# Performance work log

Hardware: AMD Instinct MI355X
Metric: run time of the kernel (lower is better)

Reference implementation:

```python
import jax, jax.numpy as jnp
import numpy as np

B, N, C, H = 8, 1024, 768, 12
DH = C // H


def setup_inputs() -> dict:
    key = jax.random.key(0)
    k1, k2, k3, k4 = jax.random.split(key, 4)
    x = jax.random.normal(k1, (B, N, C), dtype=jnp.float32)
    mask = jax.random.randint(k2, (B, N), 0, 2, dtype=jnp.int32)
    # torch Linear weights stored transposed; build directly as (in, out)
    w_qkv = jax.random.normal(k3, (C, 3 * C), dtype=jnp.float32) * (C ** -0.5)
    w_proj = jax.random.normal(k4, (C, C), dtype=jnp.float32) * (C ** -0.5)
    b_proj = jnp.zeros((C,), dtype=jnp.float32)
    return {"x": x, "mask": mask, "w_qkv": w_qkv, "w_proj": w_proj, "b_proj": b_proj}


def reference(x, mask, w_qkv, w_proj, b_proj):
    scale = DH ** -0.5
    qkv = (x @ w_qkv).reshape(B, N, 3, H, DH)          # (B,N,3,H,Dh)
    q, k, v = jnp.moveaxis(qkv, 2, 0)                  # each (B,N,H,Dh)
    q = q.transpose(0, 2, 1, 3)                        # (B,H,N,Dh)
    k = k.transpose(0, 2, 1, 3)
    v = v.transpose(0, 2, 1, 3)
    attn = jnp.einsum('bhqd,bhkd->bhqk', q, k) * scale  # (B,H,N,N)
    # mask (B,N) masks key positions for all queries/heads
    attn = jnp.where(mask[:, None, None, :] != 0, -jnp.inf, attn)
    attn = jax.nn.softmax(attn, axis=-1)
    out = jnp.einsum('bhqk,bhkd->bhqd', attn, v)        # (B,H,N,Dh)
    out = out.transpose(0, 2, 1, 3).reshape(B, N, C)
    return out @ w_proj + b_proj
```

## Files before the change

### kernel.cpp

```cpp
#include <hip/hip_runtime.h>
#include <cstdint>
#include <cstddef>

#define Bb   8
#define Nn   1024
#define Ccn  768
#define Hh   12
#define DHn  64
#define Mrows (Bb * Nn)
#define N3C  (3 * Ccn)
#define BHn  (Bb * Hh)

typedef __attribute__((ext_vector_type(8))) short bf16x8;
typedef __attribute__((ext_vector_type(4))) float f32x4;

static __device__ __forceinline__ unsigned short f2bf(float f) {
    unsigned int u = __builtin_bit_cast(unsigned int, f);
    return (unsigned short)((u + 0x7FFFu + ((u >> 16) & 1u)) >> 16);
}
static __device__ __forceinline__ float bf2f(unsigned short s) {
    unsigned int u = ((unsigned int)s) << 16;
    return __builtin_bit_cast(float, u);
}
static __device__ __forceinline__ unsigned pack2bf(float a, float b) {
    unsigned ua = __builtin_bit_cast(unsigned, a) + 0x8000u;
    unsigned ub = __builtin_bit_cast(unsigned, b) + 0x8000u;
    return (ua >> 16) | (ub & 0xFFFF0000u);
}
static __device__ __forceinline__ void glds16(const void* g, void* l) {
    __builtin_amdgcn_global_load_lds((const __attribute__((address_space(1))) void*)g,
                                     (__attribute__((address_space(3))) void*)l,
                                     16, 0, 0);
}

__global__ void convert_x_mask_kernel(const float* __restrict__ x,
                                      unsigned short* __restrict__ xb,
                                      const int* __restrict__ mask,
                                      float* __restrict__ maskneg, int n8) {
    int i = blockIdx.x * blockDim.x + threadIdx.x;
    if (i < Mrows) maskneg[i] = (mask[i] != 0) ? -1.0e9f : 0.0f;
    if (i >= n8) return;
    const f32x4* xp = (const f32x4*)x;
    f32x4 a = xp[2 * i], b = xp[2 * i + 1];
    bf16x8 v;
#pragma unroll
    for (int j = 0; j < 4; ++j) {
        v[j]     = (short)f2bf(a[j]);
        v[4 + j] = (short)f2bf(b[j]);
    }
    ((bf16x8*)xb)[i] = v;
}

__global__ void transpose_w2_kernel(const float* __restrict__ Wqkv,
                                    unsigned short* __restrict__ WqkvT,
                                    const float* __restrict__ Wproj,
                                    unsigned short* __restrict__ WprojT) {
    __shared__ float tile[32][33];
    int xb = blockIdx.x;
    const float* W; unsigned short* WT; int C;
    if (xb < 72) { W = Wqkv;  WT = WqkvT;  C = N3C; }
    else         { W = Wproj; WT = WprojT; C = Ccn; xb -= 72; }
    const int R = Ccn;
    const int c0 = xb * 32, r0 = blockIdx.y * 32;
    const int tx = threadIdx.x, ty = threadIdx.y;
#pragma unroll
    for (int i = 0; i < 4; ++i)
        tile[ty + i * 8][tx] = W[(size_t)(r0 + ty + i * 8) * C + c0 + tx];
    __syncthreads();
#pragma unroll
    for (int i = 0; i < 4; ++i)
        WT[(size_t)(c0 + ty + i * 8) * R + r0 + tx] = f2bf(tile[tx][ty + i * 8]);
}

__global__ void transpose_v_kernel(const unsigned short* __restrict__ vb,
                                   unsigned short* __restrict__ vtb) {
    __shared__ unsigned short tile[32][34];
    const int bh = blockIdx.z;
    const int d0 = blockIdx.x * 32, n0 = blockIdx.y * 32;
    const int tx = threadIdx.x, ty = threadIdx.y;
    const unsigned short* src = vb + (size_t)bh * Nn * DHn;
    unsigned short* dst = vtb + (size_t)bh * DHn * Nn;
#pragma unroll
    for (int i = 0; i < 4; ++i)
        tile[ty + i * 8][tx] = src[(size_t)(n0 + ty + i * 8) * DHn + d0 + tx];
    __syncthreads();
#pragma unroll
    for (int i = 0; i < 4; ++i)
        dst[(size_t)(d0 + ty + i * 8) * Nn + n0 + tx] = tile[tx][ty + i * 8];
}

__global__ __launch_bounds__(256) void gemm_qkv_kernel(
    const unsigned short* __restrict__ A,
    const unsigned short* __restrict__ BT,
    unsigned short* __restrict__ qkvb) {
    constexpr int K = Ccn;
    const int bm = blockIdx.x, bn = blockIdx.y;
    const int t = threadIdx.x, wv = t >> 6, l = t & 63;
    const int fr = l & 15, quad = l >> 4;
    const int wm = (wv >> 1) * 64, wn = (wv & 1) * 64;
    __shared__ __align__(16) unsigned short As[128 * 32];
    __shared__ __align__(16) unsigned short Bs[128 * 32];
    const f32x4 zero = {0.f, 0.f, 0.f, 0.f};
    f32x4 acc[4][4];
#pragma unroll
    for (int i = 0; i < 4; ++i)
#pragma unroll
        for (int j = 0; j < 4; ++j) acc[i][j] = zero;

    const int srow = wv * 16 + (l >> 2);
    const int scol_dst = (l & 3) * 8;
    const int scol_src = (((l & 3) ^ ((srow >> 1) & 3)) << 3);
    const unsigned short* Ag = A + (size_t)(bm * 128 + srow) * K + scol_src;
    const unsigned short* Bg = BT + (size_t)(bn * 128 + srow) * K + scol_src;
    unsigned short* Al = &As[srow * 32 + scol_dst];
    unsigned short* Bl = &Bs[srow * 32 + scol_dst];
    const int rsw = ((fr >> 1) & 3);

    for (int k0 = 0; k0 < K; k0 += 32) {
        glds16(Ag, Al);
        glds16(Ag + (size_t)64 * K, Al + 64 * 32);
        glds16(Bg, Bl);
        glds16(Bg + (size_t)64 * K, Bl + 64 * 32);
        Ag += 32; Bg += 32;
        __syncthreads();
        bf16x8 af[4], bfv[4];
#pragma unroll
        for (int i = 0; i < 4; ++i)
            af[i] = *(const bf16x8*)&As[(wm + i * 16 + fr) * 32 + ((quad ^ rsw) << 3)];
#pragma unroll
        for (int i = 0; i < 4; ++i)
            bfv[i] = *(const bf16x8*)&Bs[(wn + i * 16 + fr) * 32 + ((quad ^ rsw) << 3)];
#pragma unroll
        for (int i = 0; i < 4; ++i)
#pragma unroll
            for (int j = 0; j < 4; ++j)
                acc[i][j] = __builtin_amdgcn_mfma_f32_16x16x32_bf16(af[i], bfv[j], acc[i][j], 0, 0, 0);
        __syncthreads();
    }
#pragma unroll
    for (int j = 0; j < 4; ++j) {
        int col = bn * 128 + wn + j * 16 + fr;
        int s = col / Ccn;
        int rem = col - s * Ccn;
        int hh = rem >> 6, d = rem & 63;
#pragma unroll
        for (int i = 0; i < 4; ++i) {
#pragma unroll
            for (int r = 0; r < 4; ++r) {
                int row = bm * 128 + wm + i * 16 + quad * 4 + r;
                int b = row >> 10, nq = row & 1023;
                qkvb[((((size_t)s * Bb + b) * Hh + hh) * Nn + nq) * DHn + d] = f2bf(acc[i][j][r]);
            }
        }
    }
}

__global__ __launch_bounds__(256) void gemm_proj_kernel(
    const unsigned short* __restrict__ A,
    const unsigned short* __restrict__ BT,
    const float* __restrict__ bias,
    float* __restrict__ out) {
    constexpr int K = Ccn;
    const int bm = blockIdx.x, bn = blockIdx.y;
    const int t = threadIdx.x, wv = t >> 6, l = t & 63;
    const int fr = l & 15, quad = l >> 4;
    const int wm = (wv >> 1) * 64, wn = (wv & 1) * 32;
    __shared__ __align__(16) unsigned short As[128 * 32];
    __shared__ __align__(16) unsigned short Bs[64 * 32];
    const f32x4 zero = {0.f, 0.f, 0.f, 0.f};
    f32x4 acc[4][2];
#pragma unroll
    for (int i = 0; i < 4; ++i)
#pragma unroll
        for (int j = 0; j < 2; ++j) acc[i][j] = zero;

    const int srow = wv * 16 + (l >> 2);
    const int scol_dst = (l & 3) * 8;
    const int scol_src = (((l & 3) ^ ((srow >> 1) & 3)) << 3);
    const unsigned short* Ag = A + (size_t)(bm * 128 + srow) * K + scol_src;
    unsigned short* Al = &As[srow * 32 + scol_dst];
    const int rB = t >> 2, cB = t & 3;
    const int bsrc = ((cB ^ ((rB >> 1) & 3)) << 3);
    const unsigned short* Bg = BT + (size_t)(bn * 64 + rB) * K + bsrc;
    unsigned short* Bl = &Bs[rB * 32 + cB * 8];
    const int rsw = ((fr >> 1) & 3);

    for (int k0 = 0; k0 < K; k0 += 32) {
        glds16(Ag, Al);
        glds16(Ag + (size_t)64 * K, Al + 64 * 32);
        glds16(Bg, Bl);
        Ag += 32; Bg += 32;
        __syncthreads();
        bf16x8 af[4], bfv[2];
#pragma unroll
        for (int i = 0; i < 4; ++i)
            af[i] = *(const bf16x8*)&As[(wm + i * 16 + fr) * 32 + ((quad ^ rsw) << 3)];
#pragma unroll
        for (int j = 0; j < 2; ++j)
            bfv[j] = *(const bf16x8*)&Bs[(wn + j * 16 + fr) * 32 + ((quad ^ rsw) << 3)];
#pragma unroll
        for (int i = 0; i < 4; ++i)
#pragma unroll
            for (int j = 0; j < 2; ++j)
                acc[i][j] = __builtin_amdgcn_mfma_f32_16x16x32_bf16(af[i], bfv[j], acc[i][j], 0, 0, 0);
        __syncthreads();
    }
#pragma unroll
    for (int j = 0; j < 2; ++j) {
        int col = bn * 64 + wn + j * 16 + fr;
        float bv = bias[col];
#pragma unroll
        for (int i = 0; i < 4; ++i) {
#pragma unroll
            for (int r = 0; r < 4; ++r) {
                int row = bm * 128 + wm + i * 16 + quad * 4 + r;
                out[(size_t)row * Ccn + col] = acc[i][j][r] + bv;
            }
        }
    }
}

__global__ __launch_bounds__(256, 3) void attn_fused(
    const unsigned short* __restrict__ qkvb,
    const unsigned short* __restrict__ vtb,
    const float* __restrict__ maskneg,
    unsigned short* __restrict__ attnb) {
    const int hb = blockIdx.x, qt = blockIdx.y;
    const int b = hb / Hh, h = hb - b * Hh;
    const int t = threadIdx.x, wv = t >> 6, l = t & 63;
    const int fr = l & 15, quad = l >> 4;
    __shared__ __align__(16) unsigned short Ks[2][64 * 64];
    __shared__ __align__(16) unsigned short VTs[2][64 * 64];
    __shared__ __align__(16) float Ms[2][64];
    __shared__ __align__(16) unsigned short Pbuf[4][16 * 72];
    const size_t bh = (size_t)b * Hh + h;
    const unsigned short* Qg = qkvb + bh * (Nn * DHn);
    const unsigned short* Kg = qkvb + (BHn + bh) * (Nn * DHn);
    const unsigned short* Vg = vtb + bh * (DHn * Nn);
    const float* Mg = maskneg + b * Nn;
    const int q0 = qt * 128 + wv * 32;

    bf16x8 qf[2][2];
#pragma unroll
    for (int g = 0; g < 2; ++g)
#pragma unroll
        for (int c = 0; c < 2; ++c) {
            bf16x8 raw = *(const bf16x8*)&Qg[(size_t)(q0 + g * 16 + fr) * DHn + c * 32 + quad * 8];
            bf16x8 sc;
#pragma unroll
            for (int j = 0; j < 8; ++j)
                sc[j] = (short)f2bf(bf2f((unsigned short)raw[j]) * 0.125f);
            qf[g][c] = sc;
        }
    const f32x4 zero = {0.f, 0.f, 0.f, 0.f};
    f32x4 o[2][4];
    float rs[2] = {0.f, 0.f};
#pragma unroll
    for (int g = 0; g < 2; ++g)
#pragma unroll
        for (int r = 0; r < 4; ++r) o[g][r] = zero;

    const int srow = wv * 8 + (l >> 3);
    const int lincol = (l & 7) * 8;
    const int swzcol = (((l & 7) ^ (srow & 7)) << 3);

    auto stage = [&](int kbase, int bsel) {
        glds16(&Kg[(size_t)(kbase + srow) * DHn + swzcol], &Ks[bsel][srow * 64 + lincol]);
        glds16(&Kg[(size_t)(kbase + srow + 32) * DHn + swzcol], &Ks[bsel][(srow + 32) * 64 + lincol]);
        glds16(&Vg[(size_t)srow * Nn + kbase + swzcol], &VTs[bsel][srow * 64 + lincol]);
        glds16(&Vg[(size_t)(srow + 32) * Nn + kbase + swzcol], &VTs[bsel][(srow + 32) * 64 + lincol]);
        if (t < 16) glds16(&Mg[kbase + t * 4], &Ms[bsel][t * 4]);
    };
    auto compute = [&](int bsel) {
        f32x4 ci[4];
#pragma unroll
        for (int kt = 0; kt < 4; ++kt)
            ci[kt] = *(const f32x4*)&Ms[bsel][kt * 16 + quad * 4];
        bf16x8 kf0[4], kf1[4];
#pragma unroll
        for (int kt = 0; kt < 4; ++kt) {
            int rr = kt * 16 + fr, sw = rr & 7;
            kf0[kt] = *(const bf16x8*)&Ks[bsel][rr * 64 + ((quad ^ sw) << 3)];
            kf1[kt] = *(const bf16x8*)&Ks[bsel][rr * 64 + (((quad + 4) ^ sw) << 3)];
        }
        f32x4 sg[2][4];
#pragma unroll
        for (int g = 0; g < 2; ++g)
#pragma unroll
            for (int kt = 0; kt < 4; ++kt) {
                f32x4 s = __builtin_amdgcn_mfma_f32_16x16x32_bf16(kf0[kt], qf[g][0], ci[kt], 0, 0, 0);
                sg[g][kt] = __builtin_amdgcn_mfma_f32_16x16x32_bf16(kf1[kt], qf[g][1], s, 0, 0, 0);
            }
        bf16x8 vf0[4], vf1[4];
#pragma unroll
        for (int dt = 0; dt < 4; ++dt) {
            int rr = dt * 16 + fr, sw = rr & 7;
            vf0[dt] = *(const bf16x8*)&VTs[bsel][rr * 64 + ((quad ^ sw) << 3)];
            vf1[dt] = *(const bf16x8*)&VTs[bsel][rr * 64 + (((quad + 4) ^ sw) << 3)];
        }
        unsigned short* Pw = Pbuf[wv];
#pragma unroll
        for (int g = 0; g < 2; ++g) {
#pragma unroll
            for (int kt = 0; kt < 4; ++kt) {
                float p0 = __expf(sg[g][kt][0]);
                float p1 = __expf(sg[g][kt][1]);
                float p2 = __expf(sg[g][kt][2]);
                float p3 = __expf(sg[g][kt][3]);
                rs[g] += (p0 + p1) + (p2 + p3);
                uint2 pk;
                pk.x = pack2bf(p0, p1);
                pk.y = pack2bf(p2, p3);
                *(uint2*)&Pw[fr * 72 + kt * 16 + quad * 4] = pk;
            }
            bf16x8 pa0 = *(const bf16x8*)&Pw[fr * 72 + quad * 8];
            bf16x8 pa1 = *(const bf16x8*)&Pw[fr * 72 + 32 + quad * 8];
#pragma unroll
            for (int dt = 0; dt < 4; ++dt) {
                f32x4 t0 = __builtin_amdgcn_mfma_f32_16x16x32_bf16(pa0, vf0[dt], o[g][dt], 0, 0, 0);
                o[g][dt] = __builtin_amdgcn_mfma_f32_16x16x32_bf16(pa1, vf1[dt], t0, 0, 0, 0);
            }
        }
    };

    stage(0, 0);
    __syncthreads();
    for (int r = 0; r < 16; ++r) {
        if (r < 15) stage((r + 1) * 64, (r + 1) & 1);
        compute(r & 1);
        __syncthreads();
    }
#pragma unroll
    for (int g = 0; g < 2; ++g) {
        float r2 = rs[g] + __shfl_xor(rs[g], 16, 64);
        float rfull = r2 + __shfl_xor(r2, 32, 64);
        float inv[4];
#pragma unroll
        for (int r = 0; r < 4; ++r) {
            float lv = __shfl(rfull, quad * 4 + r, 64);
            inv[r] = (lv > 0.f) ? 1.0f / lv : 0.f;
        }
#pragma unroll
        for (int dt = 0; dt < 4; ++dt)
#pragma unroll
            for (int r = 0; r < 4; ++r) {
                int q = q0 + g * 16 + quad * 4 + r;
                attnb[((size_t)(b * Nn + q) * Hh + h) * DHn + dt * 16 + fr] = f2bf(o[g][dt][r] * inv[r]);
            }
    }
}

#define OFF_XB     0u
#define OFF_WQKVT  12582912u
#define OFF_WPROJT 16121856u
#define OFF_MASKB  17301504u
#define OFF_QKVB   17334272u
#define OFF_VTB    55083008u
#define OFF_ATTNB  67665920u

extern "C" void kernel_launch(void* const* d_in, const int* in_sizes, int n_in,
                              void* d_out, int out_size, void* d_ws, size_t ws_size,
                              hipStream_t stream) {
    const float* x      = (const float*)d_in[0];
    const int*   mask   = (const int*)d_in[1];
    const float* w_qkv  = (const float*)d_in[2];
    const float* w_proj = (const float*)d_in[3];
    const float* b_proj = (const float*)d_in[4];
    float* out = (float*)d_out;
    char* ws = (char*)d_ws;
    unsigned short* xb     = (unsigned short*)(ws + OFF_XB);
    unsigned short* wqkvT  = (unsigned short*)(ws + OFF_WQKVT);
    unsigned short* wprojT = (unsigned short*)(ws + OFF_WPROJT);
    float*          maskng = (float*)(ws + OFF_MASKB);
    unsigned short* qkvb   = (unsigned short*)(ws + OFF_QKVB);
    unsigned short* vtb    = (unsigned short*)(ws + OFF_VTB);
    unsigned short* attnb  = (unsigned short*)(ws + OFF_ATTNB);

    convert_x_mask_kernel<<<dim3(3072), dim3(256), 0, stream>>>(x, xb, mask, maskng, Mrows * Ccn / 8);
    transpose_w2_kernel<<<dim3(96, 24), dim3(32, 8), 0, stream>>>(w_qkv, wqkvT, w_proj, wprojT);
    gemm_qkv_kernel<<<dim3(Mrows / 128, N3C / 128), dim3(256), 0, stream>>>(xb, wqkvT, qkvb);
    transpose_v_kernel<<<dim3(DHn / 32, Nn / 32, BHn), dim3(32, 8), 0, stream>>>(
        qkvb + (size_t)2 * BHn * Nn * DHn, vtb);
    attn_fused<<<dim3(BHn, Nn / 128), dim3(256), 0, stream>>>(qkvb, vtb, maskng, attnb);
    gemm_proj_kernel<<<dim3(Mrows / 128, Ccn / 64), dim3(256), 0, stream>>>(attnb, wprojT, b_proj, out);
}
```

Measured before the change: 192.4 us.

## Double-buffer LDS tiles in both GEMMs and merge prep kernels into one launch

Both bf16 GEMMs now keep two LDS buffers per operand. The async global-to-LDS load for the next K-slice is issued before the MFMA work on the current slice, so memory latency can overlap with compute and only one barrier per iteration remains. The x/mask conversion and the weight transpose/convert kernels are merged into a single launch to save one kernel launch. The cost is twice the LDS per GEMM block, which may lower occupancy.

```diff
diff --git a/kernel.cpp b/kernel.cpp
--- a/kernel.cpp
+++ b/kernel.cpp
@@ -33,36 +33,38 @@
                                      16, 0, 0);
 }
 
-__global__ void convert_x_mask_kernel(const float* __restrict__ x,
-                                      unsigned short* __restrict__ xb,
-                                      const int* __restrict__ mask,
-                                      float* __restrict__ maskneg, int n8) {
-    int i = blockIdx.x * blockDim.x + threadIdx.x;
-    if (i < Mrows) maskneg[i] = (mask[i] != 0) ? -1.0e9f : 0.0f;
-    if (i >= n8) return;
-    const f32x4* xp = (const f32x4*)x;
-    f32x4 a = xp[2 * i], b = xp[2 * i + 1];
-    bf16x8 v;
-#pragma unroll
-    for (int j = 0; j < 4; ++j) {
-        v[j]     = (short)f2bf(a[j]);
-        v[4 + j] = (short)f2bf(b[j]);
-    }
-    ((bf16x8*)xb)[i] = v;
-}
-
-__global__ void transpose_w2_kernel(const float* __restrict__ Wqkv,
-                                    unsigned short* __restrict__ WqkvT,
-                                    const float* __restrict__ Wproj,
-                                    unsigned short* __restrict__ WprojT) {
+__global__ void prep_kernel(const float* __restrict__ x,
+                            unsigned short* __restrict__ xb,
+                            const int* __restrict__ mask,
+                            float* __restrict__ maskneg,
+                            const float* __restrict__ Wqkv,
+                            unsigned short* __restrict__ WqkvT,
+                            const float* __restrict__ Wproj,
+                            unsigned short* __restrict__ WprojT) {
     __shared__ float tile[32][33];
-    int xb = blockIdx.x;
+    int bx = blockIdx.x;
+    if (bx < 3072) {
+        int i = bx * 256 + threadIdx.x;
+        if (i < Mrows) maskneg[i] = (mask[i] != 0) ? -1.0e9f : 0.0f;
+        const f32x4* xp = (const f32x4*)x;
+        f32x4 a = xp[2 * i], b = xp[2 * i + 1];
+        bf16x8 v;
+#pragma unroll
+        for (int j = 0; j < 4; ++j) {
+            v[j]     = (short)f2bf(a[j]);
+            v[4 + j] = (short)f2bf(b[j]);
+        }
+        ((bf16x8*)xb)[i] = v;
+        return;
+    }
+    bx -= 3072;
+    int xt = bx % 96, yt = bx / 96;
     const float* W; unsigned short* WT; int C;
-    if (xb < 72) { W = Wqkv;  WT = WqkvT;  C = N3C; }
-    else         { W = Wproj; WT = WprojT; C = Ccn; xb -= 72; }
+    if (xt < 72) { W = Wqkv;  WT = WqkvT;  C = N3C; }
+    else         { W = Wproj; WT = WprojT; C = Ccn; xt -= 72; }
     const int R = Ccn;
-    const int c0 = xb * 32, r0 = blockIdx.y * 32;
-    const int tx = threadIdx.x, ty = threadIdx.y;
+    const int c0 = xt * 32, r0 = yt * 32;
+    const int tx = threadIdx.x & 31, ty = threadIdx.x >> 5;
 #pragma unroll
     for (int i = 0; i < 4; ++i)
         tile[ty + i * 8][tx] = W[(size_t)(r0 + ty + i * 8) * C + c0 + tx];
@@ -98,8 +100,8 @@
     const int t = threadIdx.x, wv = t >> 6, l = t & 63;
     const int fr = l & 15, quad = l >> 4;
     const int wm = (wv >> 1) * 64, wn = (wv & 1) * 64;
-    __shared__ __align__(16) unsigned short As[128 * 32];
-    __shared__ __align__(16) unsigned short Bs[128 * 32];
+    __shared__ __align__(16) unsigned short As[2][128 * 32];
+    __shared__ __align__(16) unsigned short Bs[2][128 * 32];
     const f32x4 zero = {0.f, 0.f, 0.f, 0.f};
     f32x4 acc[4][4];
 #pragma unroll
@@ -112,24 +114,30 @@
     const int scol_src = (((l & 3) ^ ((srow >> 1) & 3)) << 3);
     const unsigned short* Ag = A + (size_t)(bm * 128 + srow) * K + scol_src;
     const unsigned short* Bg = BT + (size_t)(bn * 128 + srow) * K + scol_src;
-    unsigned short* Al = &As[srow * 32 + scol_dst];
-    unsigned short* Bl = &Bs[srow * 32 + scol_dst];
+    const int ldst = srow * 32 + scol_dst;
     const int rsw = ((fr >> 1) & 3);
 
-    for (int k0 = 0; k0 < K; k0 += 32) {
-        glds16(Ag, Al);
-        glds16(Ag + (size_t)64 * K, Al + 64 * 32);
-        glds16(Bg, Bl);
-        glds16(Bg + (size_t)64 * K, Bl + 64 * 32);
-        Ag += 32; Bg += 32;
-        __syncthreads();
+    auto stage = [&](int r, int bsel) {
+        const unsigned short* Ar = Ag + r * 32;
+        const unsigned short* Br = Bg + r * 32;
+        glds16(Ar, &As[bsel][ldst]);
+        glds16(Ar + (size_t)64 * K, &As[bsel][ldst + 64 * 32]);
+        glds16(Br, &Bs[bsel][ldst]);
+        glds16(Br + (size_t)64 * K, &Bs[bsel][ldst + 64 * 32]);
+    };
+    stage(0, 0);
+    __syncthreads();
+    for (int r = 0; r < 24; ++r) {
+        if (r < 23) stage(r + 1, (r + 1) & 1);
+        const unsigned short* Asb = As[r & 1];
+        const unsigned short* Bsb = Bs[r & 1];
         bf16x8 af[4], bfv[4];
 #pragma unroll
         for (int i = 0; i < 4; ++i)
-            af[i] = *(const bf16x8*)&As[(wm + i * 16 + fr) * 32 + ((quad ^ rsw) << 3)];
+            af[i] = *(const bf16x8*)&Asb[(wm + i * 16 + fr) * 32 + ((quad ^ rsw) << 3)];
 #pragma unroll
         for (int i = 0; i < 4; ++i)
-            bfv[i] = *(const bf16x8*)&Bs[(wn + i * 16 + fr) * 32 + ((quad ^ rsw) << 3)];
+            bfv[i] = *(const bf16x8*)&Bsb[(wn + i * 16 + fr) * 32 + ((quad ^ rsw) << 3)];
 #pragma unroll
         for (int i = 0; i < 4; ++i)
 #pragma unroll
@@ -165,8 +173,8 @@
     const int t = threadIdx.x, wv = t >> 6, l = t & 63;
     const int fr = l & 15, quad = l >> 4;
     const int wm = (wv >> 1) * 64, wn = (wv & 1) * 32;
-    __shared__ __align__(16) unsigned short As[128 * 32];
-    __shared__ __align__(16) unsigned short Bs[64 * 32];
+    __shared__ __align__(16) unsigned short As[2][128 * 32];
+    __shared__ __align__(16) unsigned short Bs[2][64 * 32];
     const f32x4 zero = {0.f, 0.f, 0.f, 0.f};
     f32x4 acc[4][2];
 #pragma unroll
@@ -178,26 +186,32 @@
     const int scol_dst = (l & 3) * 8;
     const int scol_src = (((l & 3) ^ ((srow >> 1) & 3)) << 3);
     const unsigned short* Ag = A + (size_t)(bm * 128 + srow) * K + scol_src;
-    unsigned short* Al = &As[srow * 32 + scol_dst];
+    const int ldstA = srow * 32 + scol_dst;
     const int rB = t >> 2, cB = t & 3;
     const int bsrc = ((cB ^ ((rB >> 1) & 3)) << 3);
     const unsigned short* Bg = BT + (size_t)(bn * 64 + rB) * K + bsrc;
-    unsigned short* Bl = &Bs[rB * 32 + cB * 8];
+    const int ldstB = rB * 32 + cB * 8;
     const int rsw = ((fr >> 1) & 3);
 
-    for (int k0 = 0; k0 < K; k0 += 32) {
-        glds16(Ag, Al);
-        glds16(Ag + (size_t)64 * K, Al + 64 * 32);
-        glds16(Bg, Bl);
-        Ag += 32; Bg += 32;
-        __syncthreads();
+    auto stage = [&](int r, int bsel) {
+        const unsigned short* Ar = Ag + r * 32;
+        glds16(Ar, &As[bsel][ldstA]);
+        glds16(Ar + (size_t)64 * K, &As[bsel][ldstA + 64 * 32]);
+        glds16(Bg + r * 32, &Bs[bsel][ldstB]);
+    };
+    stage(0, 0);
+    __syncthreads();
+    for (int r = 0; r < 24; ++r) {
+        if (r < 23) stage(r + 1, (r + 1) & 1);
+        const unsigned short* Asb = As[r & 1];
+        const unsigned short* Bsb = Bs[r & 1];
         bf16x8 af[4], bfv[2];
 #pragma unroll
         for (int i = 0; i < 4; ++i)
-            af[i] = *(const bf16x8*)&As[(wm + i * 16 + fr) * 32 + ((quad ^ rsw) << 3)];
+            af[i] = *(const bf16x8*)&Asb[(wm + i * 16 + fr) * 32 + ((quad ^ rsw) << 3)];
 #pragma unroll
         for (int j = 0; j < 2; ++j)
-            bfv[j] = *(const bf16x8*)&Bs[(wn + j * 16 + fr) * 32 + ((quad ^ rsw) << 3)];
+            bfv[j] = *(const bf16x8*)&Bsb[(wn + j * 16 + fr) * 32 + ((quad ^ rsw) << 3)];
 #pragma unroll
         for (int i = 0; i < 4; ++i)
 #pragma unroll
@@ -376,8 +390,8 @@
     unsigned short* vtb    = (unsigned short*)(ws + OFF_VTB);
     unsigned short* attnb  = (unsigned short*)(ws + OFF_ATTNB);
 
-    convert_x_mask_kernel<<<dim3(3072), dim3(256), 0, stream>>>(x, xb, mask, maskng, Mrows * Ccn / 8);
-    transpose_w2_kernel<<<dim3(96, 24), dim3(32, 8), 0, stream>>>(w_qkv, wqkvT, w_proj, wprojT);
+    prep_kernel<<<dim3(5376), dim3(256), 0, stream>>>(x, xb, mask, maskng,
+                                                      w_qkv, wqkvT, w_proj, wprojT);
     gemm_qkv_kernel<<<dim3(Mrows / 128, N3C / 128), dim3(256), 0, stream>>>(xb, wqkvT, qkvb);
     transpose_v_kernel<<<dim3(DHn / 32, Nn / 32, BHn), dim3(32, 8), 0, stream>>>(
         qkvb + (size_t)2 * BHn * Nn * DHn, vtb);
```

Measured after the change: 200.2 us. 4.1% more time.
